# Kernel tuning notes

Measured on AMD Instinct MI355X. Metric: run time of the kernel, lower is better.

## Reference

```python
import jax, jax.numpy as jnp
import numpy as np

NUM_HEADS = 16
N_QUBITS = 8  # both attention d_k and FFN qubit count
LN_EPS = 1e-5


def setup_inputs() -> dict:
    key = jax.random.key(0)
    ks = jax.random.split(key, 8)
    B, S, E, F = 8, 4096, 128, 2048
    return {
        "x": jax.random.normal(ks[0], (B, S, E), dtype=jnp.float32),
        "theta_attn": jax.random.normal(ks[1], (N_QUBITS,), dtype=jnp.float32),
        "phi_ffn": jax.random.normal(ks[2], (N_QUBITS,), dtype=jnp.float32),
        "w1": jax.random.normal(ks[3], (F, N_QUBITS), dtype=jnp.float32) * (1.0 / np.sqrt(N_QUBITS)),
        "b1": jax.random.normal(ks[4], (F,), dtype=jnp.float32) * 0.01,
        "w2": jax.random.normal(ks[5], (E, F), dtype=jnp.float32) * (1.0 / np.sqrt(F)),
        "b2": jax.random.normal(ks[6], (E,), dtype=jnp.float32) * 0.01,
        "gamma1": jnp.ones((E,), dtype=jnp.float32),
        "beta1": jnp.zeros((E,), dtype=jnp.float32),
        "gamma2": jnp.ones((E,), dtype=jnp.float32),
        "beta2": jnp.zeros((E,), dtype=jnp.float32),
    }


def _layernorm(y, g, b):
    m = jnp.mean(y, axis=-1, keepdims=True)
    v = jnp.var(y, axis=-1, keepdims=True)
    return (y - m) * jax.lax.rsqrt(v + LN_EPS) * g + b


def _quantum_attn(x, theta):
    # RX(x_k)RX(theta_k) per wire -> per-wire <Z>=cos(x_k+theta_k); CNOT chain + ring
    # maps Z_j -> Z_0..Z_j (j>=1) and Z_0 -> Z_0..Z_{n-1} (Heisenberg picture),
    # so outputs are cumulative products of cosines within each head.
    B, S, E = x.shape
    a = x.reshape(B, S, NUM_HEADS, N_QUBITS) + theta  # (B,S,H,8)
    cp = jnp.cumprod(jnp.cos(a), axis=-1)
    out = jnp.concatenate([cp[..., -1:], cp[..., 1:]], axis=-1)  # wire0 gets full product
    return out.reshape(B, S, E)


def _quantum_ffn(x, phi):
    # RY(phi_j)RX(x_j)|0> -> <Z_j> = cos(phi_j)*cos(x_j); encoder only reads first N_QUBITS feats
    return jnp.cos(phi) * jnp.cos(x[..., :N_QUBITS])  # (B,S,8)


def reference(x, theta_attn, phi_ffn, w1, b1, w2, b2, gamma1, beta1, gamma2, beta2):
    attn = _quantum_attn(x, theta_attn)
    x1 = _layernorm(x + attn, gamma1, beta1)  # dropout is identity in eval
    q = _quantum_ffn(x1, phi_ffn)
    h = jax.nn.relu(jnp.einsum('bsq,fq->bsf', q, w1) + b1)
    ffn = jnp.einsum('bsf,ef->bse', h, w2) + b2
    return _layernorm(x1 + ffn, gamma2, beta2)
```

## Files before the change

### kernel.cpp

```cpp
#include <hip/hip_runtime.h>
#include <hip/hip_bf16.h>

typedef __attribute__((ext_vector_type(8))) short short8;
typedef __attribute__((ext_vector_type(4))) float f32x4;
typedef __attribute__((ext_vector_type(4))) int int4v;

#define LN_EPS 1e-5f

__device__ __forceinline__ unsigned short bf16rn(float f) {
    unsigned int u = __builtin_bit_cast(unsigned int, f);
    u = u + 0x7fffu + ((u >> 16) & 1u);
    return (unsigned short)(u >> 16);
}

__device__ __forceinline__ unsigned cvt_pk(float lo, float hi) {
    unsigned r;
    asm("v_cvt_pk_bf16_f32 %0, %1, %2" : "=v"(r) : "v"(lo), "v"(hi));
    return r;
}

__global__ __launch_bounds__(256) void k_prep(const float* __restrict__ w2,
                                              const float* __restrict__ w1,
                                              const float* __restrict__ b1,
                                              unsigned short* __restrict__ w2b,
                                              unsigned short* __restrict__ w1p) {
    const int bid = blockIdx.x;
    if (bid < 256) {
        int i = (bid * 256 + threadIdx.x) * 4;
        float4 v = *(const float4*)(w2 + i);
        ushort4 r;
        r.x = bf16rn(v.x); r.y = bf16rn(v.y); r.z = bf16rn(v.z); r.w = bf16rn(v.w);
        *(ushort4*)(w2b + i) = r;
    } else {
        int f = (bid - 256) * 256 + threadIdx.x;
        float4 wa = *(const float4*)(w1 + (size_t)f * 8);
        float4 wb = *(const float4*)(w1 + (size_t)f * 8 + 4);
        short8 r0, r1;
        r0[0] = (short)bf16rn(wa.x); r0[1] = (short)bf16rn(wa.y);
        r0[2] = (short)bf16rn(wa.z); r0[3] = (short)bf16rn(wa.w);
        r0[4] = (short)bf16rn(wb.x); r0[5] = (short)bf16rn(wb.y);
        r0[6] = (short)bf16rn(wb.z); r0[7] = (short)bf16rn(wb.w);
        r1 = short8{0, 0, 0, 0, 0, 0, 0, 0};
        r1[0] = (short)bf16rn(b1[f]);
        short8 z = short8{0, 0, 0, 0, 0, 0, 0, 0};
        unsigned short* row = w1p + (size_t)f * 32;
        *(short8*)(row) = r0;
        *(short8*)(row + 8) = r1;
        *(short8*)(row + 16) = z;
        *(short8*)(row + 24) = z;
    }
}

__global__ __launch_bounds__(256) void k_pre(const float* __restrict__ x,
                                             const float* __restrict__ theta,
                                             const float* __restrict__ phi,
                                             const float* __restrict__ gamma1,
                                             const float* __restrict__ beta1,
                                             float* __restrict__ x1,
                                             unsigned short* __restrict__ qpad) {
    const int tid = threadIdx.x;
    const int g = tid >> 4, li = tid & 15;
    const int tok = blockIdx.x * 16 + g;

    const float* xr = x + (size_t)tok * 128 + li * 8;
    float4 va = *(const float4*)xr;
    float4 vb = *(const float4*)(xr + 4);
    float v[8] = {va.x, va.y, va.z, va.w, vb.x, vb.y, vb.z, vb.w};

    float c[8];
#pragma unroll
    for (int k = 0; k < 8; ++k) c[k] = __cosf(v[k] + theta[k]);
    float cp[8];
    cp[0] = c[0];
#pragma unroll
    for (int k = 1; k < 8; ++k) cp[k] = cp[k - 1] * c[k];

    float y[8];
    y[0] = v[0] + cp[7];
#pragma unroll
    for (int k = 1; k < 8; ++k) y[k] = v[k] + cp[k];

    float s1 = 0.f, s2 = 0.f;
#pragma unroll
    for (int k = 0; k < 8; ++k) { s1 += y[k]; s2 += y[k] * y[k]; }
#pragma unroll
    for (int m = 1; m < 16; m <<= 1) {
        s1 += __shfl_xor(s1, m);
        s2 += __shfl_xor(s2, m);
    }
    float mean = s1 * (1.f / 128.f);
    float var = s2 * (1.f / 128.f) - mean * mean;
    float rs = rsqrtf(var + LN_EPS);

    float4 ga = *(const float4*)(gamma1 + li * 8);
    float4 gb = *(const float4*)(gamma1 + li * 8 + 4);
    float4 ba = *(const float4*)(beta1 + li * 8);
    float4 bb = *(const float4*)(beta1 + li * 8 + 4);
    float gam[8] = {ga.x, ga.y, ga.z, ga.w, gb.x, gb.y, gb.z, gb.w};
    float bet[8] = {ba.x, ba.y, ba.z, ba.w, bb.x, bb.y, bb.z, bb.w};

    float o[8];
#pragma unroll
    for (int k = 0; k < 8; ++k) o[k] = (y[k] - mean) * rs * gam[k] + bet[k];

    float* x1r = x1 + (size_t)tok * 128 + li * 8;
    *(float4*)x1r = make_float4(o[0], o[1], o[2], o[3]);
    *(float4*)(x1r + 4) = make_float4(o[4], o[5], o[6], o[7]);

    if (li == 0) {
        short8 qr;
#pragma unroll
        for (int k = 0; k < 8; ++k)
            qr[k] = (short)bf16rn(__cosf(phi[k]) * __cosf(o[k]));
        *(short8*)(qpad + (size_t)tok * 32) = qr;
    } else if (li < 4) {
        short8 z = short8{0, 0, 0, 0, 0, 0, 0, 0};
        if (li == 1) z[0] = (short)0x3F80;
        *(short8*)(qpad + (size_t)tok * 32 + li * 8) = z;
    }
}

__global__ __launch_bounds__(512, 2) void k_ffn(const float* __restrict__ x1,
                                                const unsigned short* __restrict__ qpad,
                                                const unsigned short* __restrict__ w2b,
                                                const unsigned short* __restrict__ w1p,
                                                const float* __restrict__ b2,
                                                const float* __restrict__ g2,
                                                const float* __restrict__ be2,
                                                float* __restrict__ out) {
    const int tid = threadIdx.x;
    const int wv = tid >> 6;
    const int kh = wv >> 2;
    const int sub = wv & 3;
    const int nh = sub & 1;
    const int mw = sub >> 1;
    const int lane = tid & 63;
    const int li = lane & 15;
    const int lg = lane >> 4;
    const int Tb = blockIdx.x * 128;
    const int lt0 = mw * 64;
    const int t0 = Tb + lt0;

    __shared__ __align__(16) unsigned short Bs[2][2][128 * 64];
    __shared__ float red[128][132];
    __shared__ float sums[128][4];

    short8 qf[4];
#pragma unroll
    for (int mt = 0; mt < 4; ++mt)
        qf[mt] = *(const short8*)(qpad + (size_t)(t0 + mt * 16 + li) * 32 + lg * 8);

    const int arow0 = (8 * (li >> 2) + (li & 3)) * 32 + lg * 8;

    f32x4 acc[4][4];
#pragma unroll
    for (int mt = 0; mt < 4; ++mt)
#pragma unroll
        for (int nt = 0; nt < 4; ++nt) acc[mt][nt] = f32x4{0.f, 0.f, 0.f, 0.f};

    const int srow = lane >> 3;
    const int scs = (lane & 7) ^ srow;

    auto stage = [&](int buf, int kb_local) {
        const int kb = kh * 1024 + kb_local;
#pragma unroll
        for (int r = 0; r < 4; ++r) {
            const int e0 = r * 32 + sub * 8;
            const unsigned short* src =
                w2b + (size_t)(e0 + srow) * 2048 + kb + scs * 8;
            unsigned short* dst = &Bs[kh][buf][e0 * 64];
            __builtin_amdgcn_global_load_lds(
                (const __attribute__((address_space(1))) unsigned int*)src,
                (__attribute__((address_space(3))) unsigned int*)dst,
                16, 0, 0);
        }
    };

    stage(0, 0);
    __syncthreads();

    const f32x4 zero4 = f32x4{0.f, 0.f, 0.f, 0.f};

    for (int kbi = 0; kbi < 16; ++kbi) {
        const int buf = kbi & 1;
        if (kbi < 15) stage(buf ^ 1, (kbi + 1) * 64);

#pragma unroll
        for (int kk = 0; kk < 2; ++kk) {
            const int f = kh * 1024 + kbi * 64 + kk * 32;

            const unsigned short* wbase = w1p + (size_t)f * 32;
            short8 A0 = *(const short8*)(wbase + arow0);
            short8 A1 = *(const short8*)(wbase + arow0 + 128);

            const int cs = (kk * 4 + lg) ^ (li & 7);
            const unsigned short* basep = &Bs[kh][buf][(nh * 64 + li) * 64 + cs * 8];
            short8 bfr[4];
#pragma unroll
            for (int nt = 0; nt < 4; ++nt)
                bfr[nt] = *(const short8*)(basep + nt * 1024);

#pragma unroll
            for (int mt = 0; mt < 4; ++mt) {
                f32x4 p0 = __builtin_amdgcn_mfma_f32_16x16x32_bf16(A0, qf[mt], zero4, 0, 0, 0);
                f32x4 p1 = __builtin_amdgcn_mfma_f32_16x16x32_bf16(A1, qf[mt], zero4, 0, 0, 0);
#pragma unroll
                for (int r = 0; r < 4; ++r) {
                    p0[r] = fmaxf(p0[r], 0.f);
                    p1[r] = fmaxf(p1[r], 0.f);
                }
                int4v ai = {(int)cvt_pk(p0[0], p0[1]), (int)cvt_pk(p0[2], p0[3]),
                            (int)cvt_pk(p1[0], p1[1]), (int)cvt_pk(p1[2], p1[3])};
                short8 a2 = __builtin_bit_cast(short8, ai);
#pragma unroll
                for (int nt = 0; nt < 4; ++nt)
                    acc[mt][nt] = __builtin_amdgcn_mfma_f32_16x16x32_bf16(a2, bfr[nt], acc[mt][nt], 0, 0, 0);
            }
        }
        __syncthreads();
    }

    if (kh == 1) {
#pragma unroll
        for (int mt = 0; mt < 4; ++mt)
#pragma unroll
            for (int nt = 0; nt < 4; ++nt)
#pragma unroll
                for (int r = 0; r < 4; ++r)
                    red[lt0 + mt * 16 + lg * 4 + r][nh * 64 + nt * 16 + li] = acc[mt][nt][r];
    }
    __syncthreads();

    float b2v[4], g2v[4], be2v[4];
    if (kh == 0) {
#pragma unroll
        for (int nt = 0; nt < 4; ++nt) {
            int e = nh * 64 + nt * 16 + li;
            b2v[nt] = b2[e]; g2v[nt] = g2[e]; be2v[nt] = be2[e];
        }
#pragma unroll
        for (int mt = 0; mt < 4; ++mt) {
#pragma unroll
            for (int r = 0; r < 4; ++r) {
                const int ltok = lt0 + mt * 16 + lg * 4 + r;
                const int tok = Tb + ltok;
                const float* x1r = x1 + (size_t)tok * 128 + nh * 64 + li;
                float s1 = 0.f, s2 = 0.f;
#pragma unroll
                for (int nt = 0; nt < 4; ++nt) {
                    float v = acc[mt][nt][r] + red[ltok][nh * 64 + nt * 16 + li] +
                              b2v[nt] + x1r[nt * 16];
                    acc[mt][nt][r] = v;
                    s1 += v; s2 += v * v;
                }
#pragma unroll
                for (int m = 1; m < 16; m <<= 1) {
                    s1 += __shfl_xor(s1, m);
                    s2 += __shfl_xor(s2, m);
                }
                if (li == 0) {
                    sums[ltok][nh * 2 + 0] = s1;
                    sums[ltok][nh * 2 + 1] = s2;
                }
            }
        }
    }
    __syncthreads();

    if (kh == 0) {
#pragma unroll
        for (int mt = 0; mt < 4; ++mt) {
#pragma unroll
            for (int r = 0; r < 4; ++r) {
                const int ltok = lt0 + mt * 16 + lg * 4 + r;
                const int tok = Tb + ltok;
                float s1 = sums[ltok][0] + sums[ltok][2];
                float s2 = sums[ltok][1] + sums[ltok][3];
                float mean = s1 * (1.f / 128.f);
                float var = s2 * (1.f / 128.f) - mean * mean;
                float rs = rsqrtf(var + LN_EPS);
                float* orow = out + (size_t)tok * 128 + nh * 64 + li;
#pragma unroll
                for (int nt = 0; nt < 4; ++nt)
                    orow[nt * 16] = (acc[mt][nt][r] - mean) * rs * g2v[nt] + be2v[nt];
            }
        }
    }
}

extern "C" void kernel_launch(void* const* d_in, const int* in_sizes, int n_in,
                              void* d_out, int out_size, void* d_ws, size_t ws_size,
                              hipStream_t stream) {
    const float* x      = (const float*)d_in[0];
    const float* theta  = (const float*)d_in[1];
    const float* phi    = (const float*)d_in[2];
    const float* w1     = (const float*)d_in[3];
    const float* b1     = (const float*)d_in[4];
    const float* w2     = (const float*)d_in[5];
    const float* b2     = (const float*)d_in[6];
    const float* gamma1 = (const float*)d_in[7];
    const float* beta1  = (const float*)d_in[8];
    const float* gamma2 = (const float*)d_in[9];
    const float* beta2  = (const float*)d_in[10];
    float* out = (float*)d_out;

    char* ws = (char*)d_ws;
    unsigned short* w2b  = (unsigned short*)ws;
    unsigned short* w1p  = (unsigned short*)(ws + (512 << 10));
    unsigned short* qpad = (unsigned short*)(ws + (1 << 20));

    k_prep<<<264, 256, 0, stream>>>(w2, w1, b1, w2b, w1p);
    k_pre<<<2048, 256, 0, stream>>>(x, theta, phi, gamma1, beta1, out, qpad);
    k_ffn<<<256, 512, 0, stream>>>(out, qpad, w2b, w1p, b2, gamma2, beta2, out);
}
```

Measured before the change: 55.79 us.

## Shrink FFN tiles to 32 tokens per block and drop split-K reduction

New measurement: 74.32 us. 33.2% more time.

```diff
diff --git a/kernel.cpp b/kernel.cpp
--- a/kernel.cpp
+++ b/kernel.cpp
@@ -120,7 +120,7 @@
     }
 }
 
-__global__ __launch_bounds__(512, 2) void k_ffn(const float* __restrict__ x1,
+__global__ __launch_bounds__(256, 4) void k_ffn(const float* __restrict__ x1,
                                                 const unsigned short* __restrict__ qpad,
                                                 const unsigned short* __restrict__ w2b,
                                                 const unsigned short* __restrict__ w1p,
@@ -130,45 +130,35 @@
                                                 float* __restrict__ out) {
     const int tid = threadIdx.x;
     const int wv = tid >> 6;
-    const int kh = wv >> 2;
-    const int sub = wv & 3;
-    const int nh = sub & 1;
-    const int mw = sub >> 1;
+    const int nh = wv & 1;
+    const int mw = wv >> 1;
     const int lane = tid & 63;
     const int li = lane & 15;
     const int lg = lane >> 4;
-    const int Tb = blockIdx.x * 128;
-    const int lt0 = mw * 64;
-    const int t0 = Tb + lt0;
-
-    __shared__ __align__(16) unsigned short Bs[2][2][128 * 64];
-    __shared__ float red[128][132];
-    __shared__ float sums[128][4];
-
-    short8 qf[4];
-#pragma unroll
-    for (int mt = 0; mt < 4; ++mt)
-        qf[mt] = *(const short8*)(qpad + (size_t)(t0 + mt * 16 + li) * 32 + lg * 8);
+    const int Tb = blockIdx.x * 32;
+    const int t0 = Tb + mw * 16;
+
+    __shared__ __align__(16) unsigned short Bs[2][128 * 64];
+    __shared__ float sums[32][4];
+
+    short8 qf = *(const short8*)(qpad + (size_t)(t0 + li) * 32 + lg * 8);
 
     const int arow0 = (8 * (li >> 2) + (li & 3)) * 32 + lg * 8;
 
-    f32x4 acc[4][4];
-#pragma unroll
-    for (int mt = 0; mt < 4; ++mt)
-#pragma unroll
-        for (int nt = 0; nt < 4; ++nt) acc[mt][nt] = f32x4{0.f, 0.f, 0.f, 0.f};
+    f32x4 acc[4];
+#pragma unroll
+    for (int nt = 0; nt < 4; ++nt) acc[nt] = f32x4{0.f, 0.f, 0.f, 0.f};
 
     const int srow = lane >> 3;
     const int scs = (lane & 7) ^ srow;
 
-    auto stage = [&](int buf, int kb_local) {
-        const int kb = kh * 1024 + kb_local;
+    auto stage = [&](int buf, int kb) {
 #pragma unroll
         for (int r = 0; r < 4; ++r) {
-            const int e0 = r * 32 + sub * 8;
+            const int e0 = r * 32 + wv * 8;
             const unsigned short* src =
                 w2b + (size_t)(e0 + srow) * 2048 + kb + scs * 8;
-            unsigned short* dst = &Bs[kh][buf][e0 * 64];
+            unsigned short* dst = &Bs[buf][e0 * 64];
             __builtin_amdgcn_global_load_lds(
                 (const __attribute__((address_space(1))) unsigned int*)src,
                 (__attribute__((address_space(3))) unsigned int*)dst,
@@ -181,110 +171,86 @@
 
     const f32x4 zero4 = f32x4{0.f, 0.f, 0.f, 0.f};
 
-    for (int kbi = 0; kbi < 16; ++kbi) {
+    for (int kbi = 0; kbi < 32; ++kbi) {
         const int buf = kbi & 1;
-        if (kbi < 15) stage(buf ^ 1, (kbi + 1) * 64);
+        if (kbi < 31) stage(buf ^ 1, (kbi + 1) * 64);
 
 #pragma unroll
         for (int kk = 0; kk < 2; ++kk) {
-            const int f = kh * 1024 + kbi * 64 + kk * 32;
+            const int f = kbi * 64 + kk * 32;
 
             const unsigned short* wbase = w1p + (size_t)f * 32;
             short8 A0 = *(const short8*)(wbase + arow0);
             short8 A1 = *(const short8*)(wbase + arow0 + 128);
 
             const int cs = (kk * 4 + lg) ^ (li & 7);
-            const unsigned short* basep = &Bs[kh][buf][(nh * 64 + li) * 64 + cs * 8];
+            const unsigned short* basep = &Bs[buf][(nh * 64 + li) * 64 + cs * 8];
             short8 bfr[4];
 #pragma unroll
             for (int nt = 0; nt < 4; ++nt)
                 bfr[nt] = *(const short8*)(basep + nt * 1024);
 
-#pragma unroll
-            for (int mt = 0; mt < 4; ++mt) {
-                f32x4 p0 = __builtin_amdgcn_mfma_f32_16x16x32_bf16(A0, qf[mt], zero4, 0, 0, 0);
-                f32x4 p1 = __builtin_amdgcn_mfma_f32_16x16x32_bf16(A1, qf[mt], zero4, 0, 0, 0);
-#pragma unroll
-                for (int r = 0; r < 4; ++r) {
-                    p0[r] = fmaxf(p0[r], 0.f);
-                    p1[r] = fmaxf(p1[r], 0.f);
-                }
-                int4v ai = {(int)cvt_pk(p0[0], p0[1]), (int)cvt_pk(p0[2], p0[3]),
-                            (int)cvt_pk(p1[0], p1[1]), (int)cvt_pk(p1[2], p1[3])};
-                short8 a2 = __builtin_bit_cast(short8, ai);
-#pragma unroll
-                for (int nt = 0; nt < 4; ++nt)
-                    acc[mt][nt] = __builtin_amdgcn_mfma_f32_16x16x32_bf16(a2, bfr[nt], acc[mt][nt], 0, 0, 0);
+            f32x4 p0 = __builtin_amdgcn_mfma_f32_16x16x32_bf16(A0, qf, zero4, 0, 0, 0);
+            f32x4 p1 = __builtin_amdgcn_mfma_f32_16x16x32_bf16(A1, qf, zero4, 0, 0, 0);
+#pragma unroll
+            for (int r = 0; r < 4; ++r) {
+                p0[r] = fmaxf(p0[r], 0.f);
+                p1[r] = fmaxf(p1[r], 0.f);
             }
+            int4v ai = {(int)cvt_pk(p0[0], p0[1]), (int)cvt_pk(p0[2], p0[3]),
+                        (int)cvt_pk(p1[0], p1[1]), (int)cvt_pk(p1[2], p1[3])};
+            short8 a2 = __builtin_bit_cast(short8, ai);
+#pragma unroll
+            for (int nt = 0; nt < 4; ++nt)
+                acc[nt] = __builtin_amdgcn_mfma_f32_16x16x32_bf16(a2, bfr[nt], acc[nt], 0, 0, 0);
         }
         __syncthreads();
     }
 
-    if (kh == 1) {
-#pragma unroll
-        for (int mt = 0; mt < 4; ++mt)
-#pragma unroll
-            for (int nt = 0; nt < 4; ++nt)
-#pragma unroll
-                for (int r = 0; r < 4; ++r)
-                    red[lt0 + mt * 16 + lg * 4 + r][nh * 64 + nt * 16 + li] = acc[mt][nt][r];
+    float b2v[4], g2v[4], be2v[4];
+#pragma unroll
+    for (int nt = 0; nt < 4; ++nt) {
+        int e = nh * 64 + nt * 16 + li;
+        b2v[nt] = b2[e]; g2v[nt] = g2[e]; be2v[nt] = be2[e];
+    }
+
+#pragma unroll
+    for (int r = 0; r < 4; ++r) {
+        const int ltok = mw * 16 + lg * 4 + r;
+        const int tok = Tb + ltok;
+        const float* x1r = x1 + (size_t)tok * 128 + nh * 64 + li;
+        float s1 = 0.f, s2 = 0.f;
+#pragma unroll
+        for (int nt = 0; nt < 4; ++nt) {
+            float v = acc[nt][r] + b2v[nt] + x1r[nt * 16];
+            acc[nt][r] = v;
+            s1 += v; s2 += v * v;
+        }
+#pragma unroll
+        for (int m = 1; m < 16; m <<= 1) {
+            s1 += __shfl_xor(s1, m);
+            s2 += __shfl_xor(s2, m);
+        }
+        if (li == 0) {
+            sums[ltok][nh * 2 + 0] = s1;
+            sums[ltok][nh * 2 + 1] = s2;
+        }
     }
     __syncthreads();
 
-    float b2v[4], g2v[4], be2v[4];
-    if (kh == 0) {
-#pragma unroll
-        for (int nt = 0; nt < 4; ++nt) {
-            int e = nh * 64 + nt * 16 + li;
-            b2v[nt] = b2[e]; g2v[nt] = g2[e]; be2v[nt] = be2[e];
-        }
-#pragma unroll
-        for (int mt = 0; mt < 4; ++mt) {
-#pragma unroll
-            for (int r = 0; r < 4; ++r) {
-                const int ltok = lt0 + mt * 16 + lg * 4 + r;
-                const int tok = Tb + ltok;
-                const float* x1r = x1 + (size_t)tok * 128 + nh * 64 + li;
-                float s1 = 0.f, s2 = 0.f;
-#pragma unroll
-                for (int nt = 0; nt < 4; ++nt) {
-                    float v = acc[mt][nt][r] + red[ltok][nh * 64 + nt * 16 + li] +
-                              b2v[nt] + x1r[nt * 16];
-                    acc[mt][nt][r] = v;
-                    s1 += v; s2 += v * v;
-                }
-#pragma unroll
-                for (int m = 1; m < 16; m <<= 1) {
-                    s1 += __shfl_xor(s1, m);
-                    s2 += __shfl_xor(s2, m);
-                }
-                if (li == 0) {
-                    sums[ltok][nh * 2 + 0] = s1;
-                    sums[ltok][nh * 2 + 1] = s2;
-                }
-            }
-        }
-    }
-    __syncthreads();
-
-    if (kh == 0) {
-#pragma unroll
-        for (int mt = 0; mt < 4; ++mt) {
-#pragma unroll
-            for (int r = 0; r < 4; ++r) {
-                const int ltok = lt0 + mt * 16 + lg * 4 + r;
-                const int tok = Tb + ltok;
-                float s1 = sums[ltok][0] + sums[ltok][2];
-                float s2 = sums[ltok][1] + sums[ltok][3];
-                float mean = s1 * (1.f / 128.f);
-                float var = s2 * (1.f / 128.f) - mean * mean;
-                float rs = rsqrtf(var + LN_EPS);
-                float* orow = out + (size_t)tok * 128 + nh * 64 + li;
-#pragma unroll
-                for (int nt = 0; nt < 4; ++nt)
-                    orow[nt * 16] = (acc[mt][nt][r] - mean) * rs * g2v[nt] + be2v[nt];
-            }
-        }
+#pragma unroll
+    for (int r = 0; r < 4; ++r) {
+        const int ltok = mw * 16 + lg * 4 + r;
+        const int tok = Tb + ltok;
+        float s1 = sums[ltok][0] + sums[ltok][2];
+        float s2 = sums[ltok][1] + sums[ltok][3];
+        float mean = s1 * (1.f / 128.f);
+        float var = s2 * (1.f / 128.f) - mean * mean;
+        float rs = rsqrtf(var + LN_EPS);
+        float* orow = out + (size_t)tok * 128 + nh * 64 + li;
+#pragma unroll
+        for (int nt = 0; nt < 4; ++nt)
+            orow[nt * 16] = (acc[nt][r] - mean) * rs * g2v[nt] + be2v[nt];
     }
 }
 
@@ -311,5 +277,5 @@
 
     k_prep<<<264, 256, 0, stream>>>(w2, w1, b1, w2b, w1p);
     k_pre<<<2048, 256, 0, stream>>>(x, theta, phi, gamma1, beta1, out, qpad);
-    k_ffn<<<256, 512, 0, stream>>>(out, qpad, w2b, w1p, b2, gamma2, beta2, out);
-}
+    k_ffn<<<1024, 256, 0, stream>>>(out, qpad, w2b, w1p, b2, gamma2, beta2, out);
+}
```
